# Kernel optimization log

Measured on AMD Instinct MI355X. Metric: run time of the kernel, lower is better.

## Reference

```python
import jax, jax.numpy as jnp
import numpy as np

NUM_UPDATES = 4

def setup_inputs() -> dict:
    key = jax.random.key(0)
    ks = jax.random.split(key, 14)
    N, E = 1024, 64
    s1, sE, s2E = 1.0, 1.0 / np.sqrt(E), 1.0 / np.sqrt(2 * E)
    inp = {
        'nodes_features': jax.random.normal(ks[0], (1, N), jnp.float32),
        'nodes_cost': jax.random.uniform(ks[1], (N, N), jnp.float32),
        'W1': jax.random.normal(ks[2], (E, 1), jnp.float32) * s1,
        'b1': jax.random.normal(ks[3], (E,), jnp.float32) * s1,
        'W2': jax.random.normal(ks[4], (E, E), jnp.float32) * sE,
        'b2': jax.random.normal(ks[5], (E,), jnp.float32) * sE,
        'W4': jax.random.normal(ks[6], (E, 1), jnp.float32) * s1,
        'b4': jax.random.normal(ks[7], (E,), jnp.float32) * s1,
        'W5': jax.random.normal(ks[8], (1, 2 * E), jnp.float32) * s2E,
        'b5': jax.random.normal(ks[9], (1,), jnp.float32) * s2E,
        'W6': jax.random.normal(ks[10], (E, E), jnp.float32) * sE,
        'b6': jax.random.normal(ks[11], (E,), jnp.float32) * sE,
        'W7': jax.random.normal(ks[12], (E, E), jnp.float32) * sE,
        'b7': jax.random.normal(ks[13], (E,), jnp.float32) * sE,
    }
    return inp

def reference(nodes_features, nodes_cost, W1, b1, W2, b2, W4, b4, W5, b5, W6, b6, W7, b7):
    x = nodes_features.T                      # (N, 1) per-node feature
    N = x.shape[0]
    E = W1.shape[0]
    # vector1 per node (constant across updates): linear1(x_v)
    V1 = x @ W1.T + b1                        # (N, E)
    # vector3 per node (constant across updates):
    # sum_i relu(cost[i, v] * w4 + b4)  -> elementwise over (N, N, E), memory-bound
    w4 = W4[:, 0]                             # (E,)
    V3 = jax.nn.relu(nodes_cost[:, :, None] * w4[None, None, :] + b4).sum(axis=0)  # (N, E)
    base = V1 + V3                            # (N, E)

    # Synchronous updates: new_emb[v] = relu(base[v] + linear2(old_emb.sum(0)))
    def step(emb, _):
        v2 = emb.sum(axis=0) @ W2.T + b2      # (E,) shared across nodes
        return jax.nn.relu(base + v2[None, :]), None

    emb0 = jnp.zeros((N, E), dtype=x.dtype)
    emb, _ = jax.lax.scan(step, emb0, None, length=NUM_UPDATES)

    # Q(v) = linear5(relu(concat(linear6(sum emb), linear7(emb[v]))))
    s = emb.sum(axis=0)                       # (E,)
    h1 = s @ W6.T + b6                        # (E,) shared
    h2 = emb @ W7.T + b7                      # (N, E)
    h = jax.nn.relu(jnp.concatenate([jnp.broadcast_to(h1, (N, E)), h2], axis=1))  # (N, 2E)
    q = h @ W5.T + b5                         # (N, 1)
    return q
```

## Files before the change

kernel.cpp:

```cpp
#include <hip/hip_runtime.h>

#define NN 1024
#define EE 64

__global__ __launch_bounds__(256) void k1a_part(
    const float* __restrict__ cost,
    const float* __restrict__ w4, const float* __restrict__ b4,
    float* __restrict__ partial)
{
    const int it = blockIdx.x;
    const int jc = blockIdx.y;
    const int jspan = NN / gridDim.y;
    const int tid = threadIdx.x;
    const int il = tid & 31;
    const int eg = tid >> 5;
    const int i = it * 32 + il;
    const int j0 = jc * jspan;

    float w4v[8], b4v[8];
#pragma unroll
    for (int ee = 0; ee < 8; ++ee) {
        w4v[ee] = w4[eg * 8 + ee];
        b4v[ee] = b4[eg * 8 + ee];
    }
    float acc[8];
#pragma unroll
    for (int ee = 0; ee < 8; ++ee) acc[ee] = 0.f;

    const float* cp = cost + (size_t)j0 * NN + i;
#pragma unroll 8
    for (int jj = 0; jj < jspan; ++jj) {
        float cv = cp[(size_t)jj * NN];
#pragma unroll
        for (int ee = 0; ee < 8; ++ee)
            acc[ee] += fmaxf(fmaf(cv, w4v[ee], b4v[ee]), 0.f);
    }
    float* dst = partial + ((size_t)jc * NN + i) * EE + eg * 8;
    *(float4*)(dst)     = make_float4(acc[0], acc[1], acc[2], acc[3]);
    *(float4*)(dst + 4) = make_float4(acc[4], acc[5], acc[6], acc[7]);
}

__global__ __launch_bounds__(256) void k1b_reduce(
    const float* __restrict__ nf,
    const float* __restrict__ W1, const float* __restrict__ b1,
    const float* __restrict__ partial, int nparts,
    float* __restrict__ base)
{
    const int idx = blockIdx.x * 256 + threadIdx.x;
    const int i = idx >> 6;
    const int e = idx & 63;
    float s0 = fmaf(nf[i], W1[e], b1[e]);
    float s1 = 0.f;
#pragma unroll 4
    for (int p = 0; p + 1 < nparts; p += 2) {
        s0 += partial[(size_t)p * (NN * EE) + idx];
        s1 += partial[(size_t)(p + 1) * (NN * EE) + idx];
    }
    if (nparts & 1) s0 += partial[(size_t)(nparts - 1) * (NN * EE) + idx];
    base[idx] = s0 + s1;
}

__global__ __launch_bounds__(1024) void k23_fused(
    const float* __restrict__ base,
    const float* __restrict__ W2, const float* __restrict__ b2,
    const float* __restrict__ W5, const float* __restrict__ b5,
    const float* __restrict__ W6, const float* __restrict__ b6,
    const float* __restrict__ W7, const float* __restrict__ b7,
    float* __restrict__ q)
{
    __shared__ float W2L[64 * 65];
    __shared__ float W7L[64 * 65];
    __shared__ float sP[1024];
    __shared__ float sS[64];
    __shared__ float sV[64];
    __shared__ float embL[16 * 64];
    __shared__ float sC;

    const int tid = threadIdx.x;
    const int c = tid & 63;
    const int g = tid >> 6;

#pragma unroll
    for (int m = tid; m < 4096; m += 1024) {
        W2L[(m >> 6) * 65 + (m & 63)] = W2[m];
        W7L[(m >> 6) * 65 + (m & 63)] = W7[m];
    }

    float bl[64];
#pragma unroll
    for (int rr = 0; rr < 64; ++rr)
        bl[rr] = base[(size_t)(g * 64 + rr) * EE + c];

    if (tid < 64) sS[c] = 0.f;
    __syncthreads();

    for (int t = 0; t < 4; ++t) {
        if (tid < 64) {
            float v = b2[c];
#pragma unroll
            for (int k = 0; k < 64; ++k) v = fmaf(W2L[c * 65 + k], sS[k], v);
            sV[c] = v;
        }
        __syncthreads();
        float v2c = sV[c];
        float a0 = 0.f, a1 = 0.f, a2 = 0.f, a3 = 0.f;
#pragma unroll
        for (int rr = 0; rr < 64; rr += 4) {
            a0 += fmaxf(bl[rr]     + v2c, 0.f);
            a1 += fmaxf(bl[rr + 1] + v2c, 0.f);
            a2 += fmaxf(bl[rr + 2] + v2c, 0.f);
            a3 += fmaxf(bl[rr + 3] + v2c, 0.f);
        }
        sP[tid] = (a0 + a1) + (a2 + a3);
        __syncthreads();
        if (tid < 64) {
            float s = 0.f;
#pragma unroll
            for (int gg = 0; gg < 16; ++gg) s += sP[gg * 64 + c];
            sS[c] = s;
        }
        __syncthreads();
    }

    if (tid < 64) {
        float h = b6[c];
#pragma unroll
        for (int k = 0; k < 64; ++k) h = fmaf(W6[c * 64 + k], sS[k], h);
        float p = fmaxf(h, 0.f) * W5[c];
#pragma unroll
        for (int off = 32; off > 0; off >>= 1) p += __shfl_down(p, off, 64);
        if (tid == 0) sC = p;
    }

    const int i = blockIdx.x * 16 + g;
    embL[g * 64 + c] = fmaxf(base[(size_t)i * EE + c] + sV[c], 0.f);
    __syncthreads();

    float h = b7[c];
#pragma unroll
    for (int k = 0; k < 64; ++k)
        h = fmaf(embL[g * 64 + k], W7L[c * 65 + k], h);
    float p = fmaxf(h, 0.f) * W5[64 + c];
#pragma unroll
    for (int off = 32; off > 0; off >>= 1) p += __shfl_down(p, off, 64);
    if (c == 0) q[i] = p + sC + b5[0];
}

extern "C" void kernel_launch(void* const* d_in, const int* in_sizes, int n_in,
                              void* d_out, int out_size, void* d_ws, size_t ws_size,
                              hipStream_t stream)
{
    (void)in_sizes; (void)n_in; (void)out_size;
    const float* nf   = (const float*)d_in[0];
    const float* cost = (const float*)d_in[1];
    const float* W1   = (const float*)d_in[2];
    const float* b1   = (const float*)d_in[3];
    const float* W2   = (const float*)d_in[4];
    const float* b2   = (const float*)d_in[5];
    const float* w4   = (const float*)d_in[6];
    const float* b4   = (const float*)d_in[7];
    const float* W5   = (const float*)d_in[8];
    const float* b5   = (const float*)d_in[9];
    const float* W6   = (const float*)d_in[10];
    const float* b6   = (const float*)d_in[11];
    const float* W7   = (const float*)d_in[12];
    const float* b7   = (const float*)d_in[13];
    float* q = (float*)d_out;

    float* base = (float*)d_ws;
    float* part = base + (size_t)NN * EE;

    size_t fixed = (size_t)NN * EE * sizeof(float);
    size_t per_part = (size_t)NN * EE * sizeof(float);
    int nparts = 16;
    while (nparts > 1 && fixed + (size_t)nparts * per_part > ws_size) nparts >>= 1;

    dim3 g1(32, nparts);
    k1a_part<<<g1, 256, 0, stream>>>(cost, w4, b4, part);
    k1b_reduce<<<256, 256, 0, stream>>>(nf, W1, b1, part, nparts, base);
    k23_fused<<<64, 1024, 0, stream>>>(base, W2, b2, W5, b5, W6, b6, W7, b7, q);
}
```

Baseline: 32.47 us.

## Register-tile relu-sum over 4 nodes x 16 embeddings with float4 loads

The partial-sum kernel now gives each thread 4 consecutive nodes and 16 embedding channels, loaded as float4 rows, with four j-strided lanes combined by wave shuffles. This raises arithmetic per load and cuts the number of partial writes per element. The cost is a large register footprint (64 accumulators). The j split goes from 16 to 32 parts with fewer i-tiles, and the reduce kernel is vectorized to float4 with 64-thread blocks. More parts mean more partial traffic, and the 64-thread reduce blocks may underfill the GPU.

```diff
diff --git a/kernel.cpp b/kernel.cpp
--- a/kernel.cpp
+++ b/kernel.cpp
@@ -12,52 +12,84 @@
     const int jc = blockIdx.y;
     const int jspan = NN / gridDim.y;
     const int tid = threadIdx.x;
-    const int il = tid & 31;
-    const int eg = tid >> 5;
-    const int i = it * 32 + il;
-    const int j0 = jc * jspan;
-
-    float w4v[8], b4v[8];
-#pragma unroll
-    for (int ee = 0; ee < 8; ++ee) {
-        w4v[ee] = w4[eg * 8 + ee];
-        b4v[ee] = b4[eg * 8 + ee];
-    }
-    float acc[8];
-#pragma unroll
-    for (int ee = 0; ee < 8; ++ee) acc[ee] = 0.f;
-
-    const float* cp = cost + (size_t)j0 * NN + i;
-#pragma unroll 8
-    for (int jj = 0; jj < jspan; ++jj) {
-        float cv = cp[(size_t)jj * NN];
-#pragma unroll
-        for (int ee = 0; ee < 8; ++ee)
-            acc[ee] += fmaxf(fmaf(cv, w4v[ee], b4v[ee]), 0.f);
-    }
-    float* dst = partial + ((size_t)jc * NN + i) * EE + eg * 8;
-    *(float4*)(dst)     = make_float4(acc[0], acc[1], acc[2], acc[3]);
-    *(float4*)(dst + 4) = make_float4(acc[4], acc[5], acc[6], acc[7]);
-}
-
-__global__ __launch_bounds__(256) void k1b_reduce(
+    const int lane = tid & 63;
+    const int eg = tid >> 6;
+    const int i4 = lane & 15;
+    const int js = lane >> 4;
+    const int ibase = it * 64 + i4 * 4;
+
+    float w4v[16], b4v[16];
+#pragma unroll
+    for (int e = 0; e < 16; ++e) {
+        w4v[e] = w4[eg * 16 + e];
+        b4v[e] = b4[eg * 16 + e];
+    }
+
+    float acc[4][16];
+#pragma unroll
+    for (int ii = 0; ii < 4; ++ii)
+#pragma unroll
+        for (int e = 0; e < 16; ++e) acc[ii][e] = 0.f;
+
+    const float* cp = cost + (size_t)(jc * jspan + js) * NN + ibase;
+    const int iters = jspan >> 2;
+#pragma unroll 4
+    for (int t = 0; t < iters; ++t) {
+        float4 cv = *(const float4*)(cp + (size_t)4 * t * NN);
+        float c0 = cv.x, c1 = cv.y, c2 = cv.z, c3 = cv.w;
+#pragma unroll
+        for (int e = 0; e < 16; ++e) {
+            acc[0][e] += fmaxf(fmaf(c0, w4v[e], b4v[e]), 0.f);
+            acc[1][e] += fmaxf(fmaf(c1, w4v[e], b4v[e]), 0.f);
+            acc[2][e] += fmaxf(fmaf(c2, w4v[e], b4v[e]), 0.f);
+            acc[3][e] += fmaxf(fmaf(c3, w4v[e], b4v[e]), 0.f);
+        }
+    }
+
+#pragma unroll
+    for (int ii = 0; ii < 4; ++ii)
+#pragma unroll
+        for (int e = 0; e < 16; ++e) {
+            float v = acc[ii][e];
+            v += __shfl_xor(v, 16, 64);
+            v += __shfl_xor(v, 32, 64);
+            acc[ii][e] = v;
+        }
+
+    if (js == 0) {
+#pragma unroll
+        for (int ii = 0; ii < 4; ++ii) {
+            float* dst = partial + ((size_t)jc * NN + ibase + ii) * EE + eg * 16;
+#pragma unroll
+            for (int ec = 0; ec < 4; ++ec)
+                *(float4*)(dst + ec * 4) = make_float4(
+                    acc[ii][ec * 4], acc[ii][ec * 4 + 1],
+                    acc[ii][ec * 4 + 2], acc[ii][ec * 4 + 3]);
+        }
+    }
+}
+
+__global__ __launch_bounds__(64) void k1b_reduce(
     const float* __restrict__ nf,
     const float* __restrict__ W1, const float* __restrict__ b1,
     const float* __restrict__ partial, int nparts,
     float* __restrict__ base)
 {
-    const int idx = blockIdx.x * 256 + threadIdx.x;
-    const int i = idx >> 6;
-    const int e = idx & 63;
-    float s0 = fmaf(nf[i], W1[e], b1[e]);
-    float s1 = 0.f;
+    const int flat = (blockIdx.x * 64 + threadIdx.x) * 4;
+    const int i = flat >> 6;
+    const int e0 = flat & 63;
+    float4 s;
+    float xi = nf[i];
+    s.x = fmaf(xi, W1[e0],     b1[e0]);
+    s.y = fmaf(xi, W1[e0 + 1], b1[e0 + 1]);
+    s.z = fmaf(xi, W1[e0 + 2], b1[e0 + 2]);
+    s.w = fmaf(xi, W1[e0 + 3], b1[e0 + 3]);
 #pragma unroll 4
-    for (int p = 0; p + 1 < nparts; p += 2) {
-        s0 += partial[(size_t)p * (NN * EE) + idx];
-        s1 += partial[(size_t)(p + 1) * (NN * EE) + idx];
-    }
-    if (nparts & 1) s0 += partial[(size_t)(nparts - 1) * (NN * EE) + idx];
-    base[idx] = s0 + s1;
+    for (int p = 0; p < nparts; ++p) {
+        float4 v = *(const float4*)(partial + (size_t)p * (NN * EE) + flat);
+        s.x += v.x; s.y += v.y; s.z += v.z; s.w += v.w;
+    }
+    *(float4*)(base + flat) = s;
 }
 
 __global__ __launch_bounds__(1024) void k23_fused(
@@ -172,11 +204,11 @@
 
     size_t fixed = (size_t)NN * EE * sizeof(float);
     size_t per_part = (size_t)NN * EE * sizeof(float);
-    int nparts = 16;
+    int nparts = 32;
     while (nparts > 1 && fixed + (size_t)nparts * per_part > ws_size) nparts >>= 1;
 
-    dim3 g1(32, nparts);
+    dim3 g1(16, nparts);
     k1a_part<<<g1, 256, 0, stream>>>(cost, w4, b4, part);
-    k1b_reduce<<<256, 256, 0, stream>>>(nf, W1, b1, part, nparts, base);
+    k1b_reduce<<<256, 64, 0, stream>>>(nf, W1, b1, part, nparts, base);
     k23_fused<<<64, 1024, 0, stream>>>(base, W2, b2, W5, b5, W6, b6, W7, b7, q);
 }
```

Result: slower. 38.49 us (+18.5%).
